# Performance work log

Hardware: AMD Instinct MI355X
Metric: run time of the kernel (lower is better)

## Reference

```python
import jax, jax.numpy as jnp
import numpy as np
import itertools

FS, C_SOUND, NMICS, NTDOAS, MAX_TAU, TRACKS = 24000, 343, 4, 6, 6, 5
B, T, TR, NCLS = 64, 500, 5, 13
NLOGIT = 2 * MAX_TAU + 1  # 13 TDOA classes
IGNORE = -100
_PAIRS = np.array([(m1, m2) for m1 in range(NMICS) for m2 in range(m1 + 1, NMICS)])  # [6,2]
_PERMS = np.array(list(itertools.permutations(range(TRACKS))))  # [120,5]


def _mic_locs():
    coords = [[0.042, 45, 35], [0.042, -45, -35], [0.042, 135, -35], [0.042, -135, 35]]
    locs = []
    for rad, azi, ele in coords:
        azi, ele = np.deg2rad(azi), np.deg2rad(ele)
        locs.append([rad * np.cos(azi) * np.cos(ele), rad * np.sin(azi) * np.cos(ele), rad * np.sin(ele)])
    return np.array(locs, dtype=np.float32)


def setup_inputs() -> dict:
    key = jax.random.key(0)
    k1, k2, k3, k4 = jax.random.split(key, 4)
    pred = jax.random.normal(k1, (B, T, NLOGIT, TR, NTDOAS), dtype=jnp.float32)
    active = (jax.random.uniform(k2, (B, T, TR, NCLS)) < 0.06).astype(jnp.float32)
    doa = jax.random.normal(k3, (B, T, TR, 3, NCLS), dtype=jnp.float32)
    doa = doa / jnp.linalg.norm(doa, axis=3, keepdims=True)
    dist = jax.random.uniform(k4, (B, T, TR, NCLS), minval=1.0, maxval=5.0, dtype=jnp.float32)
    target = jnp.concatenate([active[:, :, :, None, :], doa, dist[:, :, :, None, :]], axis=3)
    return {"pred": pred, "target": target, "mic_locs": jnp.asarray(_mic_locs())}


def _tdoa_targets(target, mic_locs):
    # target: [B,T,Tr,5,C] -> int32 class targets [B,T,Tr,NTDOAS]
    Bs, Ts, Tr, _, C = target.shape
    active = target[:, :, :, 0, :] != 0                                   # [B,T,Tr,C]
    src = jnp.moveaxis(target[:, :, :, 1:4, :] * target[:, :, :, 4:5, :], 3, -1)  # [B,T,Tr,C,3]
    d = jnp.linalg.norm(src[..., None, :] - mic_locs[None, None, None, None], axis=-1)  # [B,T,Tr,C,4]
    tdoa = d[..., _PAIRS[:, 0]] - d[..., _PAIRS[:, 1]]                    # [B,T,Tr,C,6]
    cls = jnp.round(tdoa * FS / C_SOUND).astype(jnp.int32) + MAX_TAU      # in [0, 2*max_tau]
    # pack first Tr active sources (tr-major, class-minor order) into track slots
    act_flat = active.reshape(Bs, Ts, Tr * C)
    cls_flat = cls.reshape(Bs, Ts, Tr * C, NTDOAS)
    order = jnp.argsort(jnp.logical_not(act_flat).astype(jnp.int32), axis=-1, stable=True)
    sel = order[:, :, :Tr]                                                # [B,T,Tr]
    vals = jnp.take_along_axis(cls_flat, sel[..., None], axis=2)          # [B,T,Tr,6]
    slot_ok = jnp.arange(Tr)[None, None, :] < act_flat.sum(-1)[..., None]
    return jnp.where(slot_ok[..., None], vals, IGNORE)


def reference(pred, target, mic_locs):
    tdoas = _tdoa_targets(target, mic_locs)                               # [B,T,Tr,P]
    Bs, Ts, CL, Tr, P = pred.shape
    N = Bs * Ts * P
    tgt = jnp.transpose(tdoas, (0, 1, 3, 2)).reshape(N, Tr)               # [N,Tr]
    logits = jnp.transpose(pred, (0, 1, 4, 2, 3)).reshape(N, CL, Tr)      # [N,CL,Tr]
    logp = jax.nn.log_softmax(logits, axis=1)
    valid = tgt != IGNORE
    safe = jnp.where(valid, tgt, 0)
    idx = jnp.broadcast_to(safe[:, :, None], (N, Tr, Tr))
    ce = jnp.take_along_axis(logp, idx, axis=1)                           # ce[n,i,j] = logp[n, tgt[n,i], j]
    loss_mat = jnp.where(valid[:, :, None], -ce, 0.0)                     # ignore_index -> 0 loss
    cost = loss_mat[:, np.arange(Tr)[None, :], _PERMS].mean(-1)           # [N,120]
    loss = cost.min(axis=1).mean()
    best = jnp.take(jnp.asarray(_PERMS), cost.argmin(axis=1), axis=0)     # [N,Tr]
    pred_cls = logits.argmax(axis=1)                                      # [N,Tr]
    tgt_perm = jnp.take_along_axis(tgt, best, axis=1)
    vp = tgt_perm != IGNORE
    n_pred = vp.sum()
    correct = ((pred_cls == tgt_perm) & vp).sum()
    acc = jnp.where(n_pred > 0, correct / jnp.maximum(n_pred, 1), 0.0).astype(jnp.float32)
    return loss, acc
```

## Files before the change

### kernel.cpp

```cpp
#include <hip/hip_runtime.h>
#include <hip/hip_bf16.h>
#include <math.h>

#define NCELLS 32000
#define NP_ 6
#define IGN (-100)
#define CPB 8
#define NBLK (NCELLS / CPB)
#define THREADS 256

struct PermTable { int p[120][5]; };
constexpr PermTable make_perms() {
    PermTable t{};
    for (int i = 0; i < 120; ++i) {
        int avail[5] = {0, 1, 2, 3, 4};
        int rem = i;
        const int f[5] = {24, 6, 2, 1, 1};
        for (int k = 0; k < 5; ++k) {
            int d = rem / f[k];
            rem = rem % f[k];
            t.p[i][k] = avail[d];
            for (int m = d; m < 4 - k; ++m) avail[m] = avail[m + 1];
        }
    }
    return t;
}
__device__ constexpr PermTable PT = make_perms();

__global__ __launch_bounds__(THREADS) void tdoa_fused(
        const float* __restrict__ pred, const float* __restrict__ target,
        const float* __restrict__ mic,
        float* __restrict__ costp, int* __restrict__ vpp, int* __restrict__ crp) {
    __shared__ int cnt[CPB][5];
    __shared__ int scls[CPB][NP_][5];
    const int j = threadIdx.x;
    const int blk = blockIdx.x;

    float fl[13];
    const int cellS = j / 5, trS = j - cellS * 5;
    const float* __restrict__ tg =
        target + (size_t)(blk * CPB + (cellS < CPB ? cellS : 0)) * 325 + trS * 65;
    if (j < CPB * 5) {
#pragma unroll
        for (int c = 0; c < 13; ++c) fl[c] = tg[c];
        int mycnt = 0;
#pragma unroll
        for (int c = 0; c < 13; ++c) mycnt += (fl[c] != 0.0f) ? 1 : 0;
        cnt[cellS][trS] = mycnt;
    }
    __syncthreads();
    if (j < CPB * 5) {
        int base = 0, total = 0;
#pragma unroll
        for (int t = 0; t < 5; ++t) {
            int v = cnt[cellS][t];
            total += v;
            if (t < trS) base += v;
        }
        if (trS == 0) {
            for (int s = (total < 5 ? total : 5); s < 5; ++s)
#pragma unroll
                for (int p = 0; p < 6; ++p) scls[cellS][p][s] = IGN;
        }
        float mx[4], my[4], mz[4];
#pragma unroll
        for (int m = 0; m < 4; ++m) {
            mx[m] = mic[m * 3 + 0];
            my[m] = mic[m * 3 + 1];
            mz[m] = mic[m * 3 + 2];
        }
        int slot = base;
#pragma unroll
        for (int c = 0; c < 13; ++c) {
            if (fl[c] != 0.0f) {
                if (slot < 5) {
                    float dist = tg[52 + c];
                    float sx = tg[13 + c] * dist;
                    float sy = tg[26 + c] * dist;
                    float sz = tg[39 + c] * dist;
                    float d[4];
#pragma unroll
                    for (int m = 0; m < 4; ++m) {
                        float dx = sx - mx[m], dy = sy - my[m], dz = sz - mz[m];
                        d[m] = sqrtf(dx * dx + dy * dy + dz * dz);
                    }
                    const int Q0[6] = {0, 0, 0, 1, 1, 2};
                    const int Q1[6] = {1, 2, 3, 2, 3, 3};
#pragma unroll
                    for (int q = 0; q < 6; ++q) {
                        float td = (d[Q0[q]] - d[Q1[q]]) * (24000.0f / 343.0f);
                        int cls = (int)rintf(td) + 6;
                        cls = cls < 0 ? 0 : (cls > 12 ? 12 : cls);
                        scls[cellS][q][slot] = cls;
                    }
                }
                ++slot;
            }
        }
    }
    __syncthreads();

    const int wave = j >> 6, lane = j & 63;
    float rc = 0.0f;
    int rv = 0, rr = 0;
    if (lane < 60) {
        const int grp = lane / 5, tr = lane - grp * 5;
        const int g = wave * 12 + grp;
        const int cellL = g / NP_, p = g - cellL * NP_;
        const float* __restrict__ L =
            pred + (size_t)(blk * CPB + cellL) * 390 + p;

        float v[13];
#pragma unroll
        for (int c = 0; c < 13; ++c) v[c] = L[c * 30 + tr * 6];
        float m = v[0];
        int am = 0;
#pragma unroll
        for (int c = 1; c < 13; ++c) {
            if (v[c] > m) { m = v[c]; am = c; }
        }
        float s = 0.0f;
#pragma unroll
        for (int c = 0; c < 13; ++c) s += __expf(v[c] - m);
        const float lse = m + __logf(s);

        float lmc[5];
#pragma unroll
        for (int slot = 0; slot < 5; ++slot) {
            int tcs = scls[cellL][p][slot];
            bool val = (tcs != IGN);
            int tcc = val ? tcs : 0;
            float gl = L[tcc * 30 + tr * 6];
            lmc[slot] = val ? (lse - gl) : 0.0f;
        }

        const int gb5 = grp * 5;
        float lmf[5][5];
#pragma unroll
        for (int slot = 0; slot < 5; ++slot)
#pragma unroll
            for (int t = 0; t < 5; ++t)
                lmf[slot][t] = __shfl(lmc[slot], gb5 + t, 64);

        float best = 1e30f;
        int bi = 0;
#pragma unroll
        for (int i = 0; i < 120; ++i) {
            float c = lmf[0][PT.p[i][0]] + lmf[1][PT.p[i][1]]
                    + lmf[2][PT.p[i][2]] + lmf[3][PT.p[i][3]]
                    + lmf[4][PT.p[i][4]];
            if (c < best) { best = c; bi = i; }
        }
        if (tr == 0) rc = best * (1.0f / 5.0f);

        int slot = PT.p[bi][tr];
        int tc = scls[cellL][p][slot];
        if (tc != IGN) {
            rv = 1;
            rr = (am == tc) ? 1 : 0;
        }
    }

#pragma unroll
    for (int off = 32; off > 0; off >>= 1) {
        rc += __shfl_down(rc, off, 64);
        rv += __shfl_down(rv, off, 64);
        rr += __shfl_down(rr, off, 64);
    }
    __shared__ float sf[4];
    __shared__ int sv[4], sc2[4];
    if (lane == 0) { sf[wave] = rc; sv[wave] = rv; sc2[wave] = rr; }
    __syncthreads();
    if (j == 0) {
        costp[blk] = sf[0] + sf[1] + sf[2] + sf[3];
        vpp[blk]   = sv[0] + sv[1] + sv[2] + sv[3];
        crp[blk]   = sc2[0] + sc2[1] + sc2[2] + sc2[3];
    }
}

__global__ __launch_bounds__(256) void tdoa_final(
        const float* __restrict__ costp, const int* __restrict__ vpp,
        const int* __restrict__ crp, float* __restrict__ out) {
    __shared__ float sf[4];
    __shared__ int sv[4], sc[4];
    int j = threadIdx.x;
    float c = 0.0f;
    int v = 0, r = 0;
    for (int i = j; i < NBLK; i += 256) {
        c += costp[i];
        v += vpp[i];
        r += crp[i];
    }
#pragma unroll
    for (int off = 32; off > 0; off >>= 1) {
        c += __shfl_down(c, off, 64);
        v += __shfl_down(v, off, 64);
        r += __shfl_down(r, off, 64);
    }
    int wave = j >> 6, lane = j & 63;
    if (lane == 0) { sf[wave] = c; sv[wave] = v; sc[wave] = r; }
    __syncthreads();
    if (j == 0) {
        float tc = sf[0] + sf[1] + sf[2] + sf[3];
        int tv = sv[0] + sv[1] + sv[2] + sv[3];
        int trr = sc[0] + sc[1] + sc[2] + sc[3];
        out[0] = tc / (float)(NCELLS * NP_);
        out[1] = (tv > 0) ? ((float)trr / (float)tv) : 0.0f;
    }
}

extern "C" void kernel_launch(void* const* d_in, const int* in_sizes, int n_in,
                              void* d_out, int out_size, void* d_ws, size_t ws_size,
                              hipStream_t stream) {
    const float* pred   = (const float*)d_in[0];
    const float* target = (const float*)d_in[1];
    const float* mic    = (const float*)d_in[2];
    float* out = (float*)d_out;

    float* costp = (float*)d_ws;
    int*   vpp   = (int*)((char*)d_ws + NBLK * 4);
    int*   crp   = (int*)((char*)d_ws + NBLK * 8);

    tdoa_fused<<<NBLK, THREADS, 0, stream>>>(pred, target, mic, costp, vpp, crp);
    tdoa_final<<<1, 256, 0, stream>>>(costp, vpp, crp, out);
}
```

Baseline: 148.0 us.

## Split 120-permutation search across 5 lanes by first assignment

Each of the 5 lanes in a group now fixes which track takes slot 0 (its own track) and searches only the 24 permutations of the remaining four, then the group takes the minimum through shuffles. This spreads the serial 120-iteration min-search over the lanes that previously all repeated the same work. In exchange it adds shuffle reductions and a per-lane index remap. Tie-breaking still follows lexicographic permutation order because candidates are compared in increasing global index.

```diff
diff --git a/kernel.cpp b/kernel.cpp
--- a/kernel.cpp
+++ b/kernel.cpp
@@ -27,6 +27,24 @@
 }
 __device__ constexpr PermTable PT = make_perms();
 
+struct Perm4 { int p[24][4]; };
+constexpr Perm4 make_p4() {
+    Perm4 t{};
+    for (int i = 0; i < 24; ++i) {
+        int avail[4] = {0, 1, 2, 3};
+        int rem = i;
+        const int f[4] = {6, 2, 1, 1};
+        for (int k = 0; k < 4; ++k) {
+            int d = rem / f[k];
+            rem = rem % f[k];
+            t.p[i][k] = avail[d];
+            for (int m = d; m < 3 - k; ++m) avail[m] = avail[m + 1];
+        }
+    }
+    return t;
+}
+__device__ constexpr Perm4 P4 = make_p4();
+
 __global__ __launch_bounds__(THREADS) void tdoa_fused(
         const float* __restrict__ pred, const float* __restrict__ target,
         const float* __restrict__ mic,
@@ -135,25 +153,42 @@
         }
 
         const int gb5 = grp * 5;
-        float lmf[5][5];
-#pragma unroll
-        for (int slot = 0; slot < 5; ++slot)
+        float lmf_[4][5];
+#pragma unroll
+        for (int sl = 1; sl <= 4; ++sl)
 #pragma unroll
             for (int t = 0; t < 5; ++t)
-                lmf[slot][t] = __shfl(lmc[slot], gb5 + t, 64);
-
+                lmf_[sl - 1][t] = __shfl(lmc[sl], gb5 + t, 64);
+
+        float lm2[4][4];
+#pragma unroll
+        for (int s2 = 0; s2 < 4; ++s2)
+#pragma unroll
+            for (int mm = 0; mm < 4; ++mm)
+                lm2[s2][mm] = (mm < tr) ? lmf_[s2][mm] : lmf_[s2][mm + 1];
+
+        const float base0 = lmc[0];
         float best = 1e30f;
         int bi = 0;
 #pragma unroll
-        for (int i = 0; i < 120; ++i) {
-            float c = lmf[0][PT.p[i][0]] + lmf[1][PT.p[i][1]]
-                    + lmf[2][PT.p[i][2]] + lmf[3][PT.p[i][3]]
-                    + lmf[4][PT.p[i][4]];
+        for (int i = 0; i < 24; ++i) {
+            float c = base0 + lm2[0][P4.p[i][0]] + lm2[1][P4.p[i][1]]
+                    + lm2[2][P4.p[i][2]] + lm2[3][P4.p[i][3]];
             if (c < best) { best = c; bi = i; }
         }
-        if (tr == 0) rc = best * (1.0f / 5.0f);
-
-        int slot = PT.p[bi][tr];
+        int gl_i = tr * 24 + bi;
+
+        float gbest = 1e30f;
+        int gbi = 0;
+#pragma unroll
+        for (int t = 0; t < 5; ++t) {
+            float cb = __shfl(best, gb5 + t, 64);
+            int ib = __shfl(gl_i, gb5 + t, 64);
+            if (cb < gbest) { gbest = cb; gbi = ib; }
+        }
+        if (tr == 0) rc = gbest * (1.0f / 5.0f);
+
+        int slot = PT.p[gbi][tr];
         int tc = scls[cellL][p][slot];
         if (tc != IGN) {
             rv = 1;
```

Result: faster. 136.6 us (-7.7%).
